# Optimization experiments

Hardware: AMD Instinct MI355X
Metric: run time of the kernel (lower is better)

The kernel has to match this reference:

```python
import jax, jax.numpy as jnp
import numpy as np

B, T, M, E, H, D = 4, 1024, 1024, 1024, 16, 64
SCALE = D ** (-0.5)


def setup_inputs() -> dict:
    key = jax.random.key(0)
    ks = jax.random.split(key, 8)
    w = 0.02  # weight scale for numerical stability of softmax
    return {
        "x": jax.random.normal(ks[0], (B, T, E), jnp.float32),
        "xl_memory": jax.random.normal(ks[1], (B, M, 2, H * D), jnp.float32),
        "relative_positions": jax.random.normal(ks[2], (H, T, M + T), jnp.float32),
        "Wq": jax.random.normal(ks[3], (E, H * D), jnp.float32) * w,
        "bq": jnp.zeros((H * D,), jnp.float32),
        "Wk": jax.random.normal(ks[4], (E, H * D), jnp.float32) * w,
        "bk": jnp.zeros((H * D,), jnp.float32),
        "Wv": jax.random.normal(ks[5], (E, H * D), jnp.float32) * w,
        "bv": jnp.zeros((H * D,), jnp.float32),
        "Wo": jax.random.normal(ks[6], (H * D, E), jnp.float32) * w,
        "bo": jnp.zeros((E,), jnp.float32),
    }


def reference(x, xl_memory, relative_positions, Wq, bq, Wk, bk, Wv, bv, Wo, bo):
    b, t, _ = x.shape
    q = (x @ Wq + bq) * SCALE                     # [b, t, H*D] (scale applied to queries)
    k = x @ Wk + bk
    v = x @ Wv + bv
    k_xl = xl_memory[:, :, 0]                      # [b, m, H*D]
    v_xl = xl_memory[:, :, 1]
    m = k_xl.shape[1]
    keys = jnp.concatenate((k_xl, k), axis=1)      # [b, j, H*D], j = m + t
    values = jnp.concatenate((v_xl, v), axis=1)
    j = keys.shape[1]

    qh = q.reshape(b, t, H, D).transpose(0, 2, 1, 3)       # b h i d
    kh = keys.reshape(b, j, H, D).transpose(0, 2, 1, 3)    # b h j d
    vh = values.reshape(b, j, H, D).transpose(0, 2, 1, 3)  # b h j d

    qk = jnp.einsum("bhid,bhjd->bhij", qh, kh)
    qk = relative_positions[..., -t:, -j:] + qk
    qk = qk * SCALE                                # second scale, faithful to source
    mask = jnp.triu(jnp.ones((t, j), dtype=bool), j - t + 1)
    qk = jnp.where(mask, -jnp.inf, qk)
    attn = jax.nn.softmax(qk, axis=-1)             # dropout p=0.0 -> identity

    qkv = jnp.einsum("bhij,bhjd->bhid", attn, vh)
    qkv = qkv.transpose(0, 2, 1, 3).reshape(b, t, H * D)
    out = qkv @ Wo + bo

    kv_memories = jnp.stack((keys, values), axis=-2)  # [b, j, 2, H*D]
    kv_to_add_xl = kv_memories[:, -m:]                 # [b, m, 2, H*D]
    return out, kv_to_add_xl
```

## Files before the change

### kernel.cpp

```cpp
#include <hip/hip_runtime.h>
#include <hip/hip_bf16.h>

typedef unsigned short u16;
typedef unsigned int u32;
typedef __attribute__((ext_vector_type(8))) short short8;
typedef __attribute__((ext_vector_type(4))) float f32x4;

#define B_ 4
#define T_ 1024
#define E_ 1024
#define NH 16
#define HD 1024
#define JTOT 2048
#define SCALE 0.125f
#define LOG2E 1.44269504f

__device__ __forceinline__ u16 f2b(float f) {
  u32 x = __float_as_uint(f);
  u32 r = (x + 0x7fffu + ((x >> 16) & 1u)) >> 16;
  return (u16)r;
}
__device__ __forceinline__ u16 f2b_fast(float f) {
  return (u16)((__float_as_uint(f) + 0x8000u) >> 16);
}
__device__ __forceinline__ float b2f(u16 b) {
  return __uint_as_float((u32)b << 16);
}
__device__ __forceinline__ float fexp2(float x) {
  float r;
  asm("v_exp_f32 %0, %1" : "=v"(r) : "v"(x));
  return r;
}

__device__ __forceinline__ void gload_lds16(const void* g, void* l) {
  __builtin_amdgcn_global_load_lds((const __attribute__((address_space(1))) u32*)g,
                                   (__attribute__((address_space(3))) u32*)l, 16, 0, 0);
}

__device__ __forceinline__ short8 pack8(float4 f0, float4 f1) {
  short8 o;
  o[0] = (short)f2b(f0.x); o[1] = (short)f2b(f0.y);
  o[2] = (short)f2b(f0.z); o[3] = (short)f2b(f0.w);
  o[4] = (short)f2b(f1.x); o[5] = (short)f2b(f1.y);
  o[6] = (short)f2b(f1.z); o[7] = (short)f2b(f1.w);
  return o;
}

__global__ __launch_bounds__(256) void cvt_bf16(const float* __restrict__ in,
                                                u16* __restrict__ out, int n8) {
  int i = blockIdx.x * 256 + threadIdx.x;
  if (i >= n8) return;
  const float4* p = (const float4*)in + (size_t)i * 2;
  ((short8*)out)[i] = pack8(p[0], p[1]);
}

__global__ __launch_bounds__(256) void cvt_w4T(const float* __restrict__ Wq, const float* __restrict__ Wk,
                                               const float* __restrict__ Wv, const float* __restrict__ Wo,
                                               u16* __restrict__ wqkvT, u16* __restrict__ woT) {
  __shared__ float tile[64][65];
  const float* W;
  u16* WT;
  int z = blockIdx.z;
  if (z == 0) { W = Wq; WT = wqkvT; }
  else if (z == 1) { W = Wk; WT = wqkvT + (size_t)1024 * 1024; }
  else if (z == 2) { W = Wv; WT = wqkvT + (size_t)2048 * 1024; }
  else { W = Wo; WT = woT; }
  int t = threadIdx.x;
  int r0 = blockIdx.y * 64, c0 = blockIdx.x * 64;
#pragma unroll
  for (int i = 0; i < 16; ++i) {
    int r = i * 4 + (t >> 6), c = t & 63;
    tile[r][c] = W[(size_t)(r0 + r) * 1024 + c0 + c];
  }
  __syncthreads();
#pragma unroll
  for (int i = 0; i < 16; ++i) {
    int r = i * 4 + (t >> 6), c = t & 63;
    WT[(size_t)(c0 + r) * 1024 + r0 + c] = f2b(tile[c][r]);
  }
}

__global__ __launch_bounds__(256) void cvt_xl_k(const float* __restrict__ xl, u16* __restrict__ kt) {
  int i = blockIdx.x * 256 + threadIdx.x;
  int hd8 = i & 127, j = (i >> 7) & 1023, b = i >> 17;
  const float4* p = (const float4*)(xl + ((((size_t)b * 1024 + j) * 2 + 0) * 1024 + (size_t)hd8 * 8));
  short8 o = pack8(p[0], p[1]);
  int h = hd8 >> 3, d0 = (hd8 & 7) * 8;
  int jc = j >> 6, jl = j & 63;
  u16* dst = kt + (((size_t)(b * 16 + h) * 32 + jc) * 4096) + jl * 64 + (d0 ^ ((jl & 7) << 3));
  *(short8*)dst = o;
}

__global__ __launch_bounds__(256) void cvt_xl_vT(const float* __restrict__ xl, u16* __restrict__ vt) {
  __shared__ u16 Vl[64 * 72];
  int bx = blockIdx.x;
  int jc = bx & 15, h = (bx >> 4) & 15, b = bx >> 8;
  int t = threadIdx.x;
  int j0 = jc * 64;
#pragma unroll
  for (int it = 0; it < 2; ++it) {
    int p = t + 256 * it;
    int j = p >> 3, d8 = p & 7;
    const float4* src = (const float4*)(xl + ((((size_t)b * 1024 + j0 + j) * 2 + 1) * 1024 + h * 64 + (size_t)d8 * 8));
    *(short8*)&Vl[j * 72 + d8 * 8] = pack8(src[0], src[1]);
  }
  __syncthreads();
#pragma unroll
  for (int it = 0; it < 2; ++it) {
    int p = t + 256 * it;
    int d = p >> 3, j8 = p & 7;
    short8 o;
#pragma unroll
    for (int e = 0; e < 8; ++e) o[e] = (short)Vl[(j8 * 8 + e) * 72 + d];
    u16* dst = vt + (((size_t)(b * 16 + h) * 32 + jc) * 4096) + d * 64 + ((j8 * 8) ^ ((d & 7) << 3));
    *(short8*)dst = o;
  }
}

__global__ __launch_bounds__(256) void trans_vnew(const u16* __restrict__ vb, u16* __restrict__ vt) {
  __shared__ u16 Vl[64 * 72];
  int bx = blockIdx.x;
  int jcl = bx & 15, h = (bx >> 4) & 15, b = bx >> 8;
  int jc = 16 + jcl;
  int t = threadIdx.x;
  int t0 = jcl * 64;
#pragma unroll
  for (int it = 0; it < 2; ++it) {
    int p = t + 256 * it;
    int j = p >> 3, d8 = p & 7;
    *(short8*)&Vl[j * 72 + d8 * 8] =
        *(const short8*)&vb[((size_t)b * 1024 + t0 + j) * 1024 + h * 64 + d8 * 8];
  }
  __syncthreads();
#pragma unroll
  for (int it = 0; it < 2; ++it) {
    int p = t + 256 * it;
    int d = p >> 3, j8 = p & 7;
    short8 o;
#pragma unroll
    for (int e = 0; e < 8; ++e) o[e] = (short)Vl[(j8 * 8 + e) * 72 + d];
    u16* dst = vt + (((size_t)(b * 16 + h) * 32 + jc) * 4096) + d * 64 + ((j8 * 8) ^ ((d & 7) << 3));
    *(short8*)dst = o;
  }
}

__global__ __launch_bounds__(256) void gemm_qkv(
    const u16* __restrict__ A, const u16* __restrict__ BT,
    const float* __restrict__ b0, const float* __restrict__ b1, const float* __restrict__ b2,
    u16* __restrict__ qb, u16* __restrict__ kbp, u16* __restrict__ kt, u16* __restrict__ vb) {
  __shared__ __align__(16) u16 As[128 * 32];
  __shared__ __align__(16) u16 Bs[128 * 32];
  const int t = threadIdx.x;
  const int lane = t & 63, wv = t >> 6;
  const int wr = wv >> 1, wc = wv & 1;
  const int m0 = (blockIdx.x / 24) * 128;
  const int n0 = (blockIdx.x % 24) * 128;
  const int lr = lane & 15, lg = lane >> 4;

  f32x4 acc[4][4] = {};

  for (int kc = 0; kc < 1024; kc += 32) {
    __syncthreads();
#pragma unroll
    for (int i = 0; i < 2; ++i) {
      int p = t + 256 * i;
      gload_lds16(A + (size_t)(m0 + (p >> 2)) * 1024 + kc + (p & 3) * 8, &As[p * 8]);
    }
#pragma unroll
    for (int i = 0; i < 2; ++i) {
      int p = t + 256 * i;
      gload_lds16(BT + (size_t)(n0 + (p >> 2)) * 1024 + kc + (p & 3) * 8, &Bs[p * 8]);
    }
    __syncthreads();

    short8 af[4], bf[4];
#pragma unroll
    for (int mf = 0; mf < 4; ++mf)
      af[mf] = *(const short8*)&As[(wr * 64 + mf * 16 + lr) * 32 + lg * 8];
#pragma unroll
    for (int nf = 0; nf < 4; ++nf)
      bf[nf] = *(const short8*)&Bs[(wc * 64 + nf * 16 + lr) * 32 + lg * 8];
#pragma unroll
    for (int mf = 0; mf < 4; ++mf)
#pragma unroll
      for (int nf = 0; nf < 4; ++nf)
        acc[mf][nf] = __builtin_amdgcn_mfma_f32_16x16x32_bf16(af[mf], bf[nf], acc[mf][nf], 0, 0, 0);
  }

#pragma unroll
  for (int mf = 0; mf < 4; ++mf) {
#pragma unroll
    for (int nf = 0; nf < 4; ++nf) {
#pragma unroll
      for (int r = 0; r < 4; ++r) {
        int row = m0 + wr * 64 + mf * 16 + lg * 4 + r;
        int col = n0 + wc * 64 + nf * 16 + lr;
        float v = acc[mf][nf][r];
        int b = row >> 10, tt = row & 1023;
        if (col < 1024) {
          v += b0[col];
          qb[(size_t)row * HD + col] = f2b(v * (SCALE * SCALE * LOG2E));
        } else if (col < 2048) {
          int hd = col - 1024;
          u16 kv16 = f2b(v + b1[hd]);
          kbp[(size_t)(b * 1024 + tt) * 1024 + hd] = kv16;
          int h = hd >> 6, d = hd & 63, jl = tt & 63, jc = 16 + (tt >> 6);
          kt[(((size_t)(b * 16 + h) * 32 + jc) * 4096) + jl * 64 + (d ^ ((jl & 7) << 3))] = kv16;
        } else {
          int hd = col - 2048;
          vb[(size_t)(b * 1024 + tt) * 1024 + hd] = f2b(v + b2[hd]);
        }
      }
    }
  }
}

__global__ __launch_bounds__(256) void kv_expand(const u16* __restrict__ kbp, const u16* __restrict__ vbp,
                                                 float* __restrict__ kvout) {
  int i = blockIdx.x * 256 + threadIdx.x;
  int hd8 = i & 127, tt = (i >> 7) & 1023, b = i >> 17;
  size_t src = ((size_t)(b * 1024 + tt)) * 1024 + (size_t)hd8 * 8;
  short8 k8 = *(const short8*)&kbp[src];
  short8 v8 = *(const short8*)&vbp[src];
  float4 k0, k1, v0, v1;
#pragma unroll
  for (int e = 0; e < 4; ++e) {
    ((float*)&k0)[e] = b2f((u16)k8[e]); ((float*)&k1)[e] = b2f((u16)k8[e + 4]);
    ((float*)&v0)[e] = b2f((u16)v8[e]); ((float*)&v1)[e] = b2f((u16)v8[e + 4]);
  }
  float* kdst = kvout + (((size_t)(b * 1024 + tt) * 2 + 0) * 1024) + hd8 * 8;
  float* vdst = kvout + (((size_t)(b * 1024 + tt) * 2 + 1) * 1024) + hd8 * 8;
  ((float4*)kdst)[0] = k0; ((float4*)kdst)[1] = k1;
  ((float4*)vdst)[0] = v0; ((float4*)vdst)[1] = v1;
}

__global__ __launch_bounds__(256) void gemm_out(
    const u16* __restrict__ A, const u16* __restrict__ BT,
    const float* __restrict__ bias, float* __restrict__ outf) {
  __shared__ __align__(16) u16 As[64 * 32];
  __shared__ __align__(16) u16 Bs[128 * 32];
  const int t = threadIdx.x;
  const int lane = t & 63, wv = t >> 6;
  const int wr = wv >> 1, wc = wv & 1;
  const int m0 = (blockIdx.x >> 3) * 64;
  const int n0 = (blockIdx.x & 7) * 128;
  const int lr = lane & 15, lg = lane >> 4;

  f32x4 acc[2][4] = {};

  for (int kc = 0; kc < 1024; kc += 32) {
    __syncthreads();
    gload_lds16(A + (size_t)(m0 + (t >> 2)) * 1024 + kc + (t & 3) * 8, &As[t * 8]);
#pragma unroll
    for (int i = 0; i < 2; ++i) {
      int p = t + 256 * i;
      gload_lds16(BT + (size_t)(n0 + (p >> 2)) * 1024 + kc + (p & 3) * 8, &Bs[p * 8]);
    }
    __syncthreads();

    short8 af[2], bf[4];
#pragma unroll
    for (int mf = 0; mf < 2; ++mf)
      af[mf] = *(const short8*)&As[(wr * 32 + mf * 16 + lr) * 32 + lg * 8];
#pragma unroll
    for (int nf = 0; nf < 4; ++nf)
      bf[nf] = *(const short8*)&Bs[(wc * 64 + nf * 16 + lr) * 32 + lg * 8];
#pragma unroll
    for (int mf = 0; mf < 2; ++mf)
#pragma unroll
      for (int nf = 0; nf < 4; ++nf)
        acc[mf][nf] = __builtin_amdgcn_mfma_f32_16x16x32_bf16(af[mf], bf[nf], acc[mf][nf], 0, 0, 0);
  }

#pragma unroll
  for (int mf = 0; mf < 2; ++mf)
#pragma unroll
    for (int nf = 0; nf < 4; ++nf)
#pragma unroll
      for (int r = 0; r < 4; ++r) {
        int row = m0 + wr * 32 + mf * 16 + lg * 4 + r;
        int col = n0 + wc * 64 + nf * 16 + lr;
        outf[(size_t)row * E_ + col] = acc[mf][nf][r] + bias[col];
      }
}

__global__ __launch_bounds__(256) void attn_kernel(
    const u16* __restrict__ qb, const u16* __restrict__ kt, const u16* __restrict__ vt,
    const float* __restrict__ rel, u16* __restrict__ aout) {
  __shared__ __align__(16) u16 Ks[2][4096];
  __shared__ __align__(16) u16 Vs[2][4096];
  __shared__ __align__(16) u16 Pl[4096];
  const int bx = blockIdx.x;
  const int xcd = bx & 7, s = bx >> 3;
  const int b = s & 3, key = (s >> 2) * 8 + xcd;
  const int h = key & 15, qt = key >> 4;
  const int i0 = qt * 64;
  const int t = threadIdx.x, lane = t & 63, w = t >> 6;
  const int lr = lane & 15, lg = lane >> 4;
  const int swz = (lr & 7) << 3;
  const int psw = ((lr >> 2) & 3) << 4;
  const float RC = SCALE * LOG2E;

  const u16* ktb = kt + (size_t)(b * 16 + h) * 32 * 4096;
  const u16* vtb = vt + (size_t)(b * 16 + h) * 32 * 4096;
  const float* relbase = rel + (size_t)h * T_ * JTOT;
  const int ib = i0 + w * 16 + lg * 4;

  short8 qf[2];
#pragma unroll
  for (int kc = 0; kc < 2; ++kc)
    qf[kc] = *(const short8*)&qb[(size_t)(b * T_ + i0 + w * 16 + lr) * HD + h * 64 + kc * 32 + lg * 8];

  short8 vf5;
#pragma unroll
  for (int e = 0; e < 8; ++e) vf5[e] = (lr == 0) ? (short)0x3f80 : (short)0;

  const int nch = qt + 17;

  auto stage = [&](int buf, int jc2) {
    const u16* ksrc = ktb + (size_t)jc2 * 4096;
    const u16* vsrc = vtb + (size_t)jc2 * 4096;
    gload_lds16(ksrc + t * 8, &Ks[buf][t * 8]);
    gload_lds16(ksrc + (t + 256) * 8, &Ks[buf][(t + 256) * 8]);
    gload_lds16(vsrc + t * 8, &Vs[buf][t * 8]);
    gload_lds16(vsrc + (t + 256) * 8, &Vs[buf][(t + 256) * 8]);
  };

  auto loadrel = [&](int j0, float (&rlf)[4][4]) {
#pragma unroll
    for (int nf = 0; nf < 4; ++nf)
#pragma unroll
      for (int r = 0; r < 4; ++r)
        rlf[nf][r] = relbase[(size_t)(ib + r) * JTOT + j0 + nf * 16 + lr];
  };

  float rlA[4][4], rlB[4][4];
  stage(0, 0);
  __builtin_amdgcn_sched_barrier(0);
  loadrel(0, rlA);
  loadrel(64, rlB);

  f32x4 o[5] = {};
  float mrow[4];
#pragma unroll
  for (int r = 0; r < 4; ++r) mrow[r] = -__builtin_inff();

  int cur = 0;
  auto chunkfn = [&](int jc, float (&rlu)[4][4]) {
    asm volatile("s_waitcnt vmcnt(16)" ::: "memory");
    __builtin_amdgcn_sched_barrier(0);
    asm volatile("s_barrier" ::: "memory");
    if (jc + 1 < nch) stage(cur ^ 1, jc + 1);
    __builtin_amdgcn_sched_barrier(0);

    f32x4 s4[4] = {};
    __builtin_amdgcn_s_setprio(1);
#pragma unroll
    for (int nf = 0; nf < 4; ++nf)
#pragma unroll
      for (int kc = 0; kc < 2; ++kc) {
        short8 kf = *(const short8*)&Ks[cur][(nf * 16 + lr) * 64 + ((kc * 32 + lg * 8) ^ swz)];
        s4[nf] = __builtin_amdgcn_mfma_f32_16x16x32_bf16(qf[kc], kf, s4[nf], 0, 0, 0);
      }
    __builtin_amdgcn_s_setprio(0);

    float p[4][4], lmax[4];
    const bool domask = (jc == qt + 16);
#pragma unroll
    for (int nf = 0; nf < 4; ++nf)
#pragma unroll
      for (int r = 0; r < 4; ++r) {
        float v = fmaf(rlu[nf][r], RC, s4[nf][r]);
        if (domask && (nf * 16 + lr) > (w * 16 + lg * 4 + r)) v = -__builtin_inff();
        p[nf][r] = v;
      }
    if (jc + 2 < nch) loadrel((jc + 2) * 64, rlu);
#pragma unroll
    for (int r = 0; r < 4; ++r)
      lmax[r] = fmaxf(fmaxf(p[0][r], p[1][r]), fmaxf(p[2][r], p[3][r]));

    float need = -__builtin_inff();
#pragma unroll
    for (int r = 0; r < 4; ++r) need = fmaxf(need, lmax[r] - mrow[r]);
    const bool dores = !__all(need <= 11.0f);
    if (dores) {
      float chmax[4], sc[4];
#pragma unroll
      for (int r = 0; r < 4; ++r) chmax[r] = lmax[r];
#pragma unroll
      for (int msk = 1; msk <= 8; msk <<= 1)
#pragma unroll
        for (int r = 0; r < 4; ++r)
          chmax[r] = fmaxf(chmax[r], __shfl_xor(chmax[r], msk, 64));
#pragma unroll
      for (int r = 0; r < 4; ++r) {
        float nm = fmaxf(mrow[r], chmax[r]);
        sc[r] = fexp2(mrow[r] - nm);
        mrow[r] = nm;
      }
#pragma unroll
      for (int nf = 0; nf < 5; ++nf)
#pragma unroll
        for (int r = 0; r < 4; ++r) o[nf][r] *= sc[r];
    }

#pragma unroll
    for (int nf = 0; nf < 4; ++nf)
#pragma unroll
      for (int r = 0; r < 4; ++r) {
        float pe = fexp2(p[nf][r] - mrow[r]);
        Pl[(w * 16 + lg * 4 + r) * 64 + (((nf ^ lg) << 4) + lr)] = f2b_fast(pe);
      }

    __builtin_amdgcn_s_setprio(1);
#pragma unroll
    for (int kc = 0; kc < 2; ++kc) {
      const int pcol = kc * 32 + lg * 8;
      short8 pa = *(const short8*)&Pl[(w * 16 + lr) * 64 + (pcol ^ psw)];
#pragma unroll
      for (int nf = 0; nf < 4; ++nf) {
        short8 vf = *(const short8*)&Vs[cur][(nf * 16 + lr) * 64 + (pcol ^ swz)];
        o[nf] = __builtin_amdgcn_mfma_f32_16x16x32_bf16(pa, vf, o[nf], 0, 0, 0);
      }
      o[4] = __builtin_amdgcn_mfma_f32_16x16x32_bf16(pa, vf5, o[4], 0, 0, 0);
    }
    __builtin_amdgcn_s_setprio(0);
    cur ^= 1;
  };

  int jc = 0;
  for (; jc + 1 < nch; jc += 2) {
    chunkfn(jc, rlA);
    chunkfn(jc + 1, rlB);
  }
  if (jc < nch) chunkfn(jc, rlA);

  float inv[4];
#pragma unroll
  for (int r = 0; r < 4; ++r)
    inv[r] = 1.0f / __shfl(o[4][r], lane & 48, 64);
#pragma unroll
  for (int nf = 0; nf < 4; ++nf)
#pragma unroll
    for (int r = 0; r < 4; ++r) {
      int i = i0 + w * 16 + lg * 4 + r, d = nf * 16 + lr;
      aout[(size_t)(b * T_ + i) * HD + h * 64 + d] = f2b_fast(o[nf][r] * inv[r]);
    }
}

extern "C" void kernel_launch(void* const* d_in, const int* in_sizes, int n_in,
                              void* d_out, int out_size, void* d_ws, size_t ws_size,
                              hipStream_t stream) {
  const float* x  = (const float*)d_in[0];
  const float* xl = (const float*)d_in[1];
  const float* rel = (const float*)d_in[2];
  const float* Wq = (const float*)d_in[3];
  const float* bq = (const float*)d_in[4];
  const float* Wk = (const float*)d_in[5];
  const float* bk = (const float*)d_in[6];
  const float* Wv = (const float*)d_in[7];
  const float* bv = (const float*)d_in[8];
  const float* Wo = (const float*)d_in[9];
  const float* bo = (const float*)d_in[10];

  float* out = (float*)d_out;
  float* kvout = out + (size_t)B_ * T_ * E_;

  char* ws = (char*)d_ws;
  u16* xb    = (u16*)ws; ws += (size_t)4096 * 1024 * 2;
  u16* wqkvT = (u16*)ws; ws += (size_t)3072 * 1024 * 2;
  u16* woT   = (u16*)ws; ws += (size_t)1024 * 1024 * 2;
  u16* qbuf  = (u16*)ws; ws += (size_t)4096 * 1024 * 2;
  u16* kt    = (u16*)ws; ws += (size_t)B_ * NH * 32 * 4096 * 2;
  u16* vt    = (u16*)ws; ws += (size_t)B_ * NH * 32 * 4096 * 2;
  u16* vbn   = (u16*)ws; ws += (size_t)4096 * 1024 * 2;
  u16* kbp   = (u16*)ws; ws += (size_t)4096 * 1024 * 2;
  u16* aout  = (u16*)ws; ws += (size_t)4096 * 1024 * 2;

  cvt_bf16<<<2048, 256, 0, stream>>>(x, xb, 524288);
  cvt_w4T<<<dim3(16, 16, 4), 256, 0, stream>>>(Wq, Wk, Wv, Wo, wqkvT, woT);
  cvt_xl_k<<<2048, 256, 0, stream>>>(xl, kt);
  cvt_xl_vT<<<1024, 256, 0, stream>>>(xl, vt);

  gemm_qkv<<<32 * 24, 256, 0, stream>>>(xb, wqkvT, bq, bk, bv, qbuf, kbp, kt, vbn);
  kv_expand<<<2048, 256, 0, stream>>>(kbp, vbn, kvout);
  trans_vnew<<<1024, 256, 0, stream>>>(vbn, vt);
  attn_kernel<<<1024, 256, 0, stream>>>(qbuf, kt, vt, rel, aout);
  gemm_out<<<512, 256, 0, stream>>>(aout, woT, bo, out);
}
```

Before: 211.4 us.

## Transpose QK^T MFMA so each lane owns one query row

Swaps the MFMA operands in the score computation so each lane holds scores for a single query row across consecutive keys. The relative-position bias can then be loaded as float4 vectors instead of scalar gathers, which also allows a much smaller vmcnt wait. The row max reduces to one scalar per lane with two cross-lane shuffles, and P is written to LDS as packed bf16 pairs via v_cvt_pk_bf16_f32 using the same swizzle as K/V. In exchange, the rescale path now needs extra shuffles to redistribute scale factors into the output accumulator layout.

New measurement: 212.8 us. No clear change (+0.7%).

```diff
diff --git a/kernel.cpp b/kernel.cpp
--- a/kernel.cpp
+++ b/kernel.cpp
@@ -29,6 +29,11 @@
 __device__ __forceinline__ float fexp2(float x) {
   float r;
   asm("v_exp_f32 %0, %1" : "=v"(r) : "v"(x));
+  return r;
+}
+__device__ __forceinline__ u32 cvtpk(float lo, float hi) {
+  u32 r;
+  asm("v_cvt_pk_bf16_f32 %0, %1, %2" : "=v"(r) : "v"(lo), "v"(hi));
   return r;
 }
 
@@ -298,13 +303,12 @@
   const int t = threadIdx.x, lane = t & 63, w = t >> 6;
   const int lr = lane & 15, lg = lane >> 4;
   const int swz = (lr & 7) << 3;
-  const int psw = ((lr >> 2) & 3) << 4;
   const float RC = SCALE * LOG2E;
 
   const u16* ktb = kt + (size_t)(b * 16 + h) * 32 * 4096;
   const u16* vtb = vt + (size_t)(b * 16 + h) * 32 * 4096;
-  const float* relbase = rel + (size_t)h * T_ * JTOT;
-  const int ib = i0 + w * 16 + lg * 4;
+  const float* relrow = rel + (size_t)h * T_ * JTOT + (size_t)(i0 + w * 16 + lr) * JTOT + lg * 4;
+  const int nch = qt + 17;
 
   short8 qf[2];
 #pragma unroll
@@ -314,8 +318,6 @@
   short8 vf5;
 #pragma unroll
   for (int e = 0; e < 8; ++e) vf5[e] = (lr == 0) ? (short)0x3f80 : (short)0;
-
-  const int nch = qt + 17;
 
   auto stage = [&](int buf, int jc2) {
     const u16* ksrc = ktb + (size_t)jc2 * 4096;
@@ -326,28 +328,25 @@
     gload_lds16(vsrc + (t + 256) * 8, &Vs[buf][(t + 256) * 8]);
   };
 
-  auto loadrel = [&](int j0, float (&rlf)[4][4]) {
-#pragma unroll
-    for (int nf = 0; nf < 4; ++nf)
-#pragma unroll
-      for (int r = 0; r < 4; ++r)
-        rlf[nf][r] = relbase[(size_t)(ib + r) * JTOT + j0 + nf * 16 + lr];
+  auto loadrel = [&](int j0, float4 (&rlf)[4]) {
+#pragma unroll
+    for (int nf = 0; nf < 4; ++nf)
+      rlf[nf] = *(const float4*)(relrow + j0 + nf * 16);
   };
 
-  float rlA[4][4], rlB[4][4];
+  float4 rlA[4], rlB[4];
   stage(0, 0);
   __builtin_amdgcn_sched_barrier(0);
   loadrel(0, rlA);
   loadrel(64, rlB);
 
-  f32x4 o[5] = {};
-  float mrow[4];
-#pragma unroll
-  for (int r = 0; r < 4; ++r) mrow[r] = -__builtin_inff();
+  f32x4 o[4] = {};
+  f32x4 o5 = {};
+  float mrow = -__builtin_inff();
 
   int cur = 0;
-  auto chunkfn = [&](int jc, float (&rlu)[4][4]) {
-    asm volatile("s_waitcnt vmcnt(16)" ::: "memory");
+  auto chunkfn = [&](int jc, float4 (&rlu)[4]) {
+    asm volatile("s_waitcnt vmcnt(4)" ::: "memory");
     __builtin_amdgcn_sched_barrier(0);
     asm volatile("s_barrier" ::: "memory");
     if (jc + 1 < nch) stage(cur ^ 1, jc + 1);
@@ -360,69 +359,63 @@
 #pragma unroll
       for (int kc = 0; kc < 2; ++kc) {
         short8 kf = *(const short8*)&Ks[cur][(nf * 16 + lr) * 64 + ((kc * 32 + lg * 8) ^ swz)];
-        s4[nf] = __builtin_amdgcn_mfma_f32_16x16x32_bf16(qf[kc], kf, s4[nf], 0, 0, 0);
+        s4[nf] = __builtin_amdgcn_mfma_f32_16x16x32_bf16(kf, qf[kc], s4[nf], 0, 0, 0);
       }
     __builtin_amdgcn_s_setprio(0);
 
-    float p[4][4], lmax[4];
+    float p[4][4], lmax = -__builtin_inff();
     const bool domask = (jc == qt + 16);
 #pragma unroll
     for (int nf = 0; nf < 4; ++nf)
 #pragma unroll
       for (int r = 0; r < 4; ++r) {
-        float v = fmaf(rlu[nf][r], RC, s4[nf][r]);
-        if (domask && (nf * 16 + lr) > (w * 16 + lg * 4 + r)) v = -__builtin_inff();
+        float v = fmaf(((const float*)&rlu[nf])[r], RC, s4[nf][r]);
+        if (domask && (nf * 16 + lg * 4 + r) > (w * 16 + lr)) v = -__builtin_inff();
         p[nf][r] = v;
+        lmax = fmaxf(lmax, v);
       }
     if (jc + 2 < nch) loadrel((jc + 2) * 64, rlu);
-#pragma unroll
-    for (int r = 0; r < 4; ++r)
-      lmax[r] = fmaxf(fmaxf(p[0][r], p[1][r]), fmaxf(p[2][r], p[3][r]));
-
-    float need = -__builtin_inff();
-#pragma unroll
-    for (int r = 0; r < 4; ++r) need = fmaxf(need, lmax[r] - mrow[r]);
-    const bool dores = !__all(need <= 11.0f);
+
+    const bool dores = !__all(lmax - mrow <= 11.0f);
     if (dores) {
-      float chmax[4], sc[4];
-#pragma unroll
-      for (int r = 0; r < 4; ++r) chmax[r] = lmax[r];
-#pragma unroll
-      for (int msk = 1; msk <= 8; msk <<= 1)
-#pragma unroll
-        for (int r = 0; r < 4; ++r)
-          chmax[r] = fmaxf(chmax[r], __shfl_xor(chmax[r], msk, 64));
-#pragma unroll
-      for (int r = 0; r < 4; ++r) {
-        float nm = fmaxf(mrow[r], chmax[r]);
-        sc[r] = fexp2(mrow[r] - nm);
-        mrow[r] = nm;
-      }
-#pragma unroll
-      for (int nf = 0; nf < 5; ++nf)
-#pragma unroll
-        for (int r = 0; r < 4; ++r) o[nf][r] *= sc[r];
-    }
-
-#pragma unroll
-    for (int nf = 0; nf < 4; ++nf)
-#pragma unroll
-      for (int r = 0; r < 4; ++r) {
-        float pe = fexp2(p[nf][r] - mrow[r]);
-        Pl[(w * 16 + lg * 4 + r) * 64 + (((nf ^ lg) << 4) + lr)] = f2b_fast(pe);
-      }
+      float ch = fmaxf(lmax, __shfl_xor(lmax, 16, 64));
+      ch = fmaxf(ch, __shfl_xor(ch, 32, 64));
+      float nm = fmaxf(mrow, ch);
+      float sc = fexp2(mrow - nm);
+      mrow = nm;
+      float sco[4];
+#pragma unroll
+      for (int r = 0; r < 4; ++r) sco[r] = __shfl(sc, lg * 4 + r, 64);
+#pragma unroll
+      for (int nf = 0; nf < 4; ++nf)
+#pragma unroll
+        for (int r = 0; r < 4; ++r) o[nf][r] *= sco[r];
+#pragma unroll
+      for (int r = 0; r < 4; ++r) o5[r] *= sco[r];
+    }
+
+    {
+      u32* plrow = (u32*)&Pl[(w * 16 + lr) * 64];
+#pragma unroll
+      for (int nf = 0; nf < 4; ++nf) {
+        float e0 = fexp2(p[nf][0] - mrow), e1 = fexp2(p[nf][1] - mrow);
+        float e2 = fexp2(p[nf][2] - mrow), e3 = fexp2(p[nf][3] - mrow);
+        u32 w0 = cvtpk(e0, e1), w1 = cvtpk(e2, e3);
+        plrow[((nf * 16 + lg * 4 + 0) ^ swz) >> 1] = w0;
+        plrow[((nf * 16 + lg * 4 + 2) ^ swz) >> 1] = w1;
+      }
+    }
 
     __builtin_amdgcn_s_setprio(1);
 #pragma unroll
     for (int kc = 0; kc < 2; ++kc) {
-      const int pcol = kc * 32 + lg * 8;
-      short8 pa = *(const short8*)&Pl[(w * 16 + lr) * 64 + (pcol ^ psw)];
+      short8 pa = *(const short8*)&Pl[(w * 16 + lr) * 64 + ((kc * 32 + lg * 8) ^ swz)];
 #pragma unroll
       for (int nf = 0; nf < 4; ++nf) {
-        short8 vf = *(const short8*)&Vs[cur][(nf * 16 + lr) * 64 + (pcol ^ swz)];
+        short8 vf = *(const short8*)&Vs[cur][(nf * 16 + lr) * 64 + ((kc * 32 + lg * 8) ^ swz)];
         o[nf] = __builtin_amdgcn_mfma_f32_16x16x32_bf16(pa, vf, o[nf], 0, 0, 0);
       }
-      o[4] = __builtin_amdgcn_mfma_f32_16x16x32_bf16(pa, vf5, o[4], 0, 0, 0);
+      o5 = __builtin_amdgcn_mfma_f32_16x16x32_bf16(pa, vf5, o5, 0, 0, 0);
     }
     __builtin_amdgcn_s_setprio(0);
     cur ^= 1;
@@ -438,7 +431,7 @@
   float inv[4];
 #pragma unroll
   for (int r = 0; r < 4; ++r)
-    inv[r] = 1.0f / __shfl(o[4][r], lane & 48, 64);
+    inv[r] = 1.0f / __shfl(o5[r], lane & 48, 64);
 #pragma unroll
   for (int nf = 0; nf < 4; ++nf)
 #pragma unroll
```
